# Optimization experiments

Measured on AMD Instinct MI355X. Metric: run time of the kernel, lower is better.

## Reference

```python
import jax, jax.numpy as jnp
import numpy as np

D_MODEL = 1024
N_EXPERTS = 8
D_FF = 4096
B, S = 2, 2048
INIT_SCALE = 0.02


def setup_inputs() -> dict:
    key = jax.random.key(0)
    ks = jax.random.split(key, 8)
    x = jax.random.normal(ks[0], (B, S, D_MODEL), dtype=jnp.float32)
    gate_w = jax.random.normal(ks[1], (D_MODEL, N_EXPERTS), dtype=jnp.float32) * INIT_SCALE
    gate_b = jnp.zeros((N_EXPERTS,), dtype=jnp.float32)
    w1 = jax.random.normal(ks[2], (N_EXPERTS, D_MODEL, D_FF), dtype=jnp.float32) * INIT_SCALE
    b1 = jnp.zeros((N_EXPERTS, D_FF), dtype=jnp.float32)
    w2 = jax.random.normal(ks[3], (N_EXPERTS, D_FF, D_MODEL), dtype=jnp.float32) * INIT_SCALE
    b2 = jnp.zeros((N_EXPERTS, D_MODEL), dtype=jnp.float32)
    return {"x": x, "gate_w": gate_w, "gate_b": gate_b,
            "w1": w1, "b1": b1, "w2": w2, "b2": b2}


def reference(x, gate_w, gate_b, w1, b1, w2, b2):
    E = w1.shape[0]
    # --- Top2Router ---
    logits = x @ gate_w + gate_b                      # [B,S,E]
    scores = jax.nn.softmax(logits, axis=-1)          # [B,S,E]
    val, idx = jax.lax.top_k(scores, 2)               # [B,S,2]
    # scatter top-2 softmax values into a dense [B,S,E] dispatch mask
    dispatch = (jax.nn.one_hot(idx, E, dtype=scores.dtype) * val[..., None]).sum(axis=-2)
    expert_counts = dispatch.sum(axis=(0, 1))         # [E]
    # --- dense loop over experts (vectorized over E), masked combine ---
    # h: [B,E,S,d_ff]
    h = jax.nn.gelu(jnp.einsum('bsd,edf->besf', x, w1) + b1[None, :, None, :],
                    approximate=False)
    y = jnp.einsum('besf,efd->besd', h, w2) + b2[None, :, None, :]  # [B,E,S,D]
    out = jnp.einsum('besd,bse->bsd', y, dispatch)    # masked sum over experts
    return out, dispatch, expert_counts
```

## Files before the change

### kernel.cpp

```cpp
#include <hip/hip_runtime.h>
#include <hip/hip_bf16.h>
#include <math.h>

#define DM    1024
#define NE    8
#define DF    4096
#define NT    4096
#define RCAP  9216
#define OUT_N   (NT*DM)
#define DISP_N  (NT*NE)
#define TOTAL_OUT (OUT_N + DISP_N + NE)

typedef __attribute__((ext_vector_type(4))) float f32x4;
typedef __attribute__((ext_vector_type(8))) short bf16x8;

#define WS_CNT    0
#define WS_FILL   32
#define WS_OFFS   64
#define WS_TOK    128
#define WS_WGT    (WS_TOK + RCAP*4)
#define WS_TOPE   (WS_WGT + RCAP*4)
#define WS_TOPV   (WS_TOPE + NT*2*4)
#define WS_W1T    (((WS_TOPV + NT*2*4) + 255) & ~255ul)
#define WS_W2T    (WS_W1T + (size_t)NE*DF*DM*2)
#define WS_XG     (WS_W2T + (size_t)NE*DM*DF*2)
#define WS_H      (WS_XG  + (size_t)RCAP*DM*2)

__device__ __forceinline__ void async_copy16(const __hip_bfloat16* g, __hip_bfloat16* l) {
    __builtin_amdgcn_global_load_lds(
        (const __attribute__((address_space(1))) unsigned int*)g,
        (__attribute__((address_space(3))) unsigned int*)l, 16, 0, 0);
}

__global__ void init_kernel(float* __restrict__ out, int* __restrict__ cnt,
                            int* __restrict__ fill, int* __restrict__ tok) {
    int gid = blockIdx.x * blockDim.x + threadIdx.x;
    int stride = gridDim.x * blockDim.x;
    for (int i = gid; i < TOTAL_OUT; i += stride) out[i] = 0.0f;
    if (gid < RCAP) tok[gid] = -1;
    if (gid < NE) { cnt[gid] = 0; fill[gid] = 0; }
}

__global__ void transpose_cast(const float* __restrict__ in, __hip_bfloat16* __restrict__ outp,
                               int R, int C) {
    __shared__ float tile[32][33];
    int e = blockIdx.z;
    int c0 = blockIdx.x * 32, r0 = blockIdx.y * 32;
    const float* ib = in + (size_t)e * R * C;
    __hip_bfloat16* ob = outp + (size_t)e * R * C;
    int tx = threadIdx.x & 31, ty = threadIdx.x >> 5;
    for (int rr = ty; rr < 32; rr += 8)
        tile[rr][tx] = ib[(size_t)(r0 + rr) * C + c0 + tx];
    __syncthreads();
    for (int cc = ty; cc < 32; cc += 8)
        ob[(size_t)(c0 + cc) * R + r0 + tx] = __float2bfloat16(tile[tx][cc]);
}

__global__ void gate_kernel(const float* __restrict__ x, const float* __restrict__ gw,
                            const float* __restrict__ gb, float* __restrict__ disp,
                            float* __restrict__ counts, int* __restrict__ cnt,
                            int* __restrict__ tope, float* __restrict__ topv) {
    int t = blockIdx.x;
    int l = threadIdx.x;
    const float* xr = x + (size_t)t * DM;
    double p[NE];
    #pragma unroll
    for (int e = 0; e < NE; ++e) p[e] = 0.0;
    for (int i = 0; i < DM / 64; ++i) {
        int d = l + 64 * i;
        double xv = (double)xr[d];
        const float* gr = gw + (size_t)d * NE;
        #pragma unroll
        for (int e = 0; e < NE; ++e) p[e] += xv * (double)gr[e];
    }
    #pragma unroll
    for (int off = 32; off > 0; off >>= 1) {
        #pragma unroll
        for (int e = 0; e < NE; ++e) p[e] += __shfl_xor(p[e], off, 64);
    }
    if (l == 0) {
        double lg[NE];
        double m = -1e300;
        #pragma unroll
        for (int e = 0; e < NE; ++e) { lg[e] = p[e] + (double)gb[e]; m = fmax(m, lg[e]); }
        double s = 0.0;
        #pragma unroll
        for (int e = 0; e < NE; ++e) s += exp(lg[e] - m);
        int e1 = 0;
        #pragma unroll
        for (int e = 1; e < NE; ++e) if (lg[e] > lg[e1]) e1 = e;
        int e2 = (e1 == 0) ? 1 : 0;
        #pragma unroll
        for (int e = 0; e < NE; ++e) if (e != e1 && lg[e] > lg[e2]) e2 = e;
        float v1 = (float)(exp(lg[e1] - m) / s);
        float v2 = (float)(exp(lg[e2] - m) / s);
        float* dr = disp + (size_t)t * NE;
        #pragma unroll
        for (int e = 0; e < NE; ++e) dr[e] = 0.0f;
        dr[e1] = v1; dr[e2] = v2;
        atomicAdd(&counts[e1], v1);
        atomicAdd(&counts[e2], v2);
        atomicAdd(&cnt[e1], 1);
        atomicAdd(&cnt[e2], 1);
        tope[2 * t] = e1;     topv[2 * t] = v1;
        tope[2 * t + 1] = e2; topv[2 * t + 1] = v2;
    }
}

__global__ void scan_kernel(const int* __restrict__ cnt, int* __restrict__ offs) {
    if (threadIdx.x == 0 && blockIdx.x == 0) {
        int o = 0;
        for (int e = 0; e < NE; ++e) {
            offs[e] = o;
            o += (cnt[e] + 127) & ~127;
        }
        offs[NE] = o;
    }
}

__global__ void build_kernel(const int* __restrict__ tope, const float* __restrict__ topv,
                             const int* __restrict__ offs, int* __restrict__ fill,
                             int* __restrict__ tok, float* __restrict__ wgt) {
    int t = blockIdx.x * blockDim.x + threadIdx.x;
    if (t >= NT) return;
    #pragma unroll
    for (int s = 0; s < 2; ++s) {
        int e = tope[2 * t + s];
        int pos = atomicAdd(&fill[e], 1);
        int row = offs[e] + pos;
        tok[row] = t;
        wgt[row] = topv[2 * t + s];
    }
}

__global__ void gather_kernel(const float* __restrict__ x, const int* __restrict__ tok,
                              __hip_bfloat16* __restrict__ xg) {
    int row = blockIdx.x;
    int t = tok[row];
    if (t < 0) return;
    int i = threadIdx.x;
    const float4 v = ((const float4*)(x + (size_t)t * DM))[i];
    ushort4 o;
    o.x = __bfloat16_as_ushort(__float2bfloat16(v.x));
    o.y = __bfloat16_as_ushort(__float2bfloat16(v.y));
    o.z = __bfloat16_as_ushort(__float2bfloat16(v.z));
    o.w = __bfloat16_as_ushort(__float2bfloat16(v.w));
    ((ushort4*)(xg + (size_t)row * DM))[i] = o;
}


__global__ __launch_bounds__(256) void gemm1_kernel(
    const __hip_bfloat16* __restrict__ xg, const __hip_bfloat16* __restrict__ w1t,
    const float* __restrict__ b1, __hip_bfloat16* __restrict__ h,
    const int* __restrict__ offs, const int* __restrict__ cnt) {
    __shared__ __hip_bfloat16 As[128 * 32];
    __shared__ __hip_bfloat16 Bs[128 * 32];
    const int row0 = blockIdx.y * 128;
    const int total = offs[NE];
    if (row0 >= total) return;
    int e = 0;
    while (row0 >= offs[e + 1]) ++e;
    if (row0 >= offs[e] + cnt[e]) return;
    const int n0 = blockIdx.x * 128;
    const __hip_bfloat16* Ab = xg + (size_t)row0 * DM;
    const __hip_bfloat16* Bb = w1t + (size_t)e * DF * DM + (size_t)n0 * DM;

    const int tid = threadIdx.x, lane = tid & 63, wave = tid >> 6;
    const int wm = wave >> 1, wn = wave & 1, g = lane >> 4, r = lane & 15;
    const int c1 = tid, c2 = tid + 256;

    f32x4 acc[4][4];
    #pragma unroll
    for (int m = 0; m < 4; ++m)
        #pragma unroll
        for (int n = 0; n < 4; ++n)
            #pragma unroll
            for (int j = 0; j < 4; ++j) acc[m][n][j] = 0.0f;

    for (int k0 = 0; k0 < DM; k0 += 32) {
        async_copy16(Ab + (size_t)(c1 >> 2) * DM + k0 + (c1 & 3) * 8, As + c1 * 8);
        async_copy16(Ab + (size_t)(c2 >> 2) * DM + k0 + (c2 & 3) * 8, As + c2 * 8);
        async_copy16(Bb + (size_t)(c1 >> 2) * DM + k0 + (c1 & 3) * 8, Bs + c1 * 8);
        async_copy16(Bb + (size_t)(c2 >> 2) * DM + k0 + (c2 & 3) * 8, Bs + c2 * 8);
        __syncthreads();
        bf16x8 af[4], bfr[4];
        #pragma unroll
        for (int m = 0; m < 4; ++m)
            af[m] = *(const bf16x8*)(As + (wm * 64 + m * 16 + r) * 32 + g * 8);
        #pragma unroll
        for (int n = 0; n < 4; ++n)
            bfr[n] = *(const bf16x8*)(Bs + (wn * 64 + n * 16 + r) * 32 + g * 8);
        #pragma unroll
        for (int m = 0; m < 4; ++m)
            #pragma unroll
            for (int n = 0; n < 4; ++n)
                acc[m][n] = __builtin_amdgcn_mfma_f32_16x16x32_bf16(af[m], bfr[n], acc[m][n], 0, 0, 0);
        __syncthreads();
    }
    float bb[4];
    #pragma unroll
    for (int n = 0; n < 4; ++n) bb[n] = b1[(size_t)e * DF + n0 + wn * 64 + n * 16 + r];
    #pragma unroll
    for (int m = 0; m < 4; ++m) {
        #pragma unroll
        for (int i = 0; i < 4; ++i) {
            int rowi = row0 + wm * 64 + m * 16 + g * 4 + i;
            __hip_bfloat16* hr = h + (size_t)rowi * DF + n0 + wn * 64 + r;
            #pragma unroll
            for (int n = 0; n < 4; ++n) {
                float v = acc[m][n][i] + bb[n];
                float ge = 0.5f * v * (1.0f + erff(v * 0.70710678118654752f));
                hr[n * 16] = __float2bfloat16(ge);
            }
        }
    }
}

__global__ __launch_bounds__(256) void gemm2_kernel(
    const __hip_bfloat16* __restrict__ h, const __hip_bfloat16* __restrict__ w2t,
    const float* __restrict__ b2, float* __restrict__ out,
    const int* __restrict__ offs, const int* __restrict__ cnt,
    const int* __restrict__ tok, const float* __restrict__ wgt) {
    __shared__ __hip_bfloat16 As[128 * 32];
    __shared__ __hip_bfloat16 Bs[128 * 32];
    const int row0 = blockIdx.y * 128;
    const int total = offs[NE];
    if (row0 >= total) return;
    int e = 0;
    while (row0 >= offs[e + 1]) ++e;
    if (row0 >= offs[e] + cnt[e]) return;
    const int n0 = blockIdx.x * 128;
    const __hip_bfloat16* Ab = h + (size_t)row0 * DF;
    const __hip_bfloat16* Bb = w2t + (size_t)e * DM * DF + (size_t)n0 * DF;

    const int tid = threadIdx.x, lane = tid & 63, wave = tid >> 6;
    const int wm = wave >> 1, wn = wave & 1, g = lane >> 4, r = lane & 15;
    const int c1 = tid, c2 = tid + 256;

    f32x4 acc[4][4];
    #pragma unroll
    for (int m = 0; m < 4; ++m)
        #pragma unroll
        for (int n = 0; n < 4; ++n)
            #pragma unroll
            for (int j = 0; j < 4; ++j) acc[m][n][j] = 0.0f;

    for (int k0 = 0; k0 < DF; k0 += 32) {
        async_copy16(Ab + (size_t)(c1 >> 2) * DF + k0 + (c1 & 3) * 8, As + c1 * 8);
        async_copy16(Ab + (size_t)(c2 >> 2) * DF + k0 + (c2 & 3) * 8, As + c2 * 8);
        async_copy16(Bb + (size_t)(c1 >> 2) * DF + k0 + (c1 & 3) * 8, Bs + c1 * 8);
        async_copy16(Bb + (size_t)(c2 >> 2) * DF + k0 + (c2 & 3) * 8, Bs + c2 * 8);
        __syncthreads();
        bf16x8 af[4], bfr[4];
        #pragma unroll
        for (int m = 0; m < 4; ++m)
            af[m] = *(const bf16x8*)(As + (wm * 64 + m * 16 + r) * 32 + g * 8);
        #pragma unroll
        for (int n = 0; n < 4; ++n)
            bfr[n] = *(const bf16x8*)(Bs + (wn * 64 + n * 16 + r) * 32 + g * 8);
        #pragma unroll
        for (int m = 0; m < 4; ++m)
            #pragma unroll
            for (int n = 0; n < 4; ++n)
                acc[m][n] = __builtin_amdgcn_mfma_f32_16x16x32_bf16(af[m], bfr[n], acc[m][n], 0, 0, 0);
        __syncthreads();
    }
    float bb[4];
    #pragma unroll
    for (int n = 0; n < 4; ++n) bb[n] = b2[(size_t)e * DM + n0 + wn * 64 + n * 16 + r];
    #pragma unroll
    for (int m = 0; m < 4; ++m) {
        #pragma unroll
        for (int i = 0; i < 4; ++i) {
            int rowi = row0 + wm * 64 + m * 16 + g * 4 + i;
            int t = tok[rowi];
            if (t < 0) continue;
            float wv = wgt[rowi];
            float* orow = out + (size_t)t * DM + n0 + wn * 64 + r;
            #pragma unroll
            for (int n = 0; n < 4; ++n)
                atomicAdd(orow + n * 16, wv * (acc[m][n][i] + bb[n]));
        }
    }
}

extern "C" void kernel_launch(void* const* d_in, const int* in_sizes, int n_in,
                              void* d_out, int out_size, void* d_ws, size_t ws_size,
                              hipStream_t stream) {
    const float* x  = (const float*)d_in[0];
    const float* gw = (const float*)d_in[1];
    const float* gb = (const float*)d_in[2];
    const float* w1 = (const float*)d_in[3];
    const float* b1 = (const float*)d_in[4];
    const float* w2 = (const float*)d_in[5];
    const float* b2 = (const float*)d_in[6];

    float* out    = (float*)d_out;
    float* disp   = out + OUT_N;
    float* counts = disp + DISP_N;

    char* ws = (char*)d_ws;
    int*   cnt  = (int*)(ws + WS_CNT);
    int*   fill = (int*)(ws + WS_FILL);
    int*   offs = (int*)(ws + WS_OFFS);
    int*   tok  = (int*)(ws + WS_TOK);
    float* wgt  = (float*)(ws + WS_WGT);
    int*   tope = (int*)(ws + WS_TOPE);
    float* topv = (float*)(ws + WS_TOPV);
    __hip_bfloat16* w1t = (__hip_bfloat16*)(ws + WS_W1T);
    __hip_bfloat16* w2t = (__hip_bfloat16*)(ws + WS_W2T);
    __hip_bfloat16* xg  = (__hip_bfloat16*)(ws + WS_XG);
    __hip_bfloat16* h   = (__hip_bfloat16*)(ws + WS_H);

    init_kernel<<<4096, 256, 0, stream>>>(out, cnt, fill, tok);
    transpose_cast<<<dim3(DF / 32, DM / 32, NE), 256, 0, stream>>>(w1, w1t, DM, DF);
    transpose_cast<<<dim3(DM / 32, DF / 32, NE), 256, 0, stream>>>(w2, w2t, DF, DM);
    gate_kernel<<<NT, 64, 0, stream>>>(x, gw, gb, disp, counts, cnt, tope, topv);
    scan_kernel<<<1, 64, 0, stream>>>(cnt, offs);
    build_kernel<<<NT / 256, 256, 0, stream>>>(tope, topv, offs, fill, tok, wgt);
    gather_kernel<<<RCAP, 256, 0, stream>>>(x, tok, xg);
    gemm1_kernel<<<dim3(DF / 128, RCAP / 128), 256, 0, stream>>>(xg, w1t, b1, h, offs, cnt);
    gemm2_kernel<<<dim3(DM / 128, RCAP / 128), 256, 0, stream>>>(h, w2t, b2, out, offs, cnt, tok, wgt);
}
```

Measured before the change: 786.0 us.

## Widen weight transpose tiles, split-K gemm2, remap workgroups, use tanh GELU

The weight transpose-cast now uses 64x64 tiles, float4 loads and ushort4 stores, and converts to bf16 before writing to LDS. gemm1 and gemm2 use a 1D grid with a workgroup remap that spreads neighbouring blocks across 8 groups, likely for XCD/L2 locality. gemm2 splits K four ways and accumulates into the output with atomics, giving more blocks and parallelism at the cost of four times the atomic traffic. The exact erf GELU is replaced by the tanh approximation, which slightly changes numerics.

```diff
diff --git a/kernel.cpp b/kernel.cpp
--- a/kernel.cpp
+++ b/kernel.cpp
@@ -32,6 +32,13 @@
         (__attribute__((address_space(3))) unsigned int*)l, 16, 0, 0);
 }
 
+__device__ __forceinline__ float gelu_f(float v) {
+    float u = v * (0.7978845608028654f + 0.044715f * 0.7978845608028654f * v * v);
+    float t = __expf(2.0f * u);
+    float th = 1.0f - 2.0f / (t + 1.0f);
+    return 0.5f * v * (1.0f + th);
+}
+
 __global__ void init_kernel(float* __restrict__ out, int* __restrict__ cnt,
                             int* __restrict__ fill, int* __restrict__ tok) {
     int gid = blockIdx.x * blockDim.x + threadIdx.x;
@@ -41,19 +48,30 @@
     if (gid < NE) { cnt[gid] = 0; fill[gid] = 0; }
 }
 
-__global__ void transpose_cast(const float* __restrict__ in, __hip_bfloat16* __restrict__ outp,
-                               int R, int C) {
-    __shared__ float tile[32][33];
+__global__ __launch_bounds__(256) void transpose_cast2(const float* __restrict__ in,
+                                                       __hip_bfloat16* __restrict__ outp,
+                                                       int R, int C) {
+    __shared__ ushort tile[64][72];
     int e = blockIdx.z;
-    int c0 = blockIdx.x * 32, r0 = blockIdx.y * 32;
+    int c0 = blockIdx.x * 64, r0 = blockIdx.y * 64;
     const float* ib = in + (size_t)e * R * C;
-    __hip_bfloat16* ob = outp + (size_t)e * R * C;
-    int tx = threadIdx.x & 31, ty = threadIdx.x >> 5;
-    for (int rr = ty; rr < 32; rr += 8)
-        tile[rr][tx] = ib[(size_t)(r0 + rr) * C + c0 + tx];
+    ushort* ob = (ushort*)outp + (size_t)e * R * C;
+    int tx = threadIdx.x & 15, ty = threadIdx.x >> 4;
+    #pragma unroll
+    for (int j = 0; j < 4; ++j) {
+        int row = ty + 16 * j;
+        float4 v = *(const float4*)(ib + (size_t)(r0 + row) * C + c0 + tx * 4);
+        tile[tx * 4 + 0][row] = __bfloat16_as_ushort(__float2bfloat16(v.x));
+        tile[tx * 4 + 1][row] = __bfloat16_as_ushort(__float2bfloat16(v.y));
+        tile[tx * 4 + 2][row] = __bfloat16_as_ushort(__float2bfloat16(v.z));
+        tile[tx * 4 + 3][row] = __bfloat16_as_ushort(__float2bfloat16(v.w));
+    }
     __syncthreads();
-    for (int cc = ty; cc < 32; cc += 8)
-        ob[(size_t)(c0 + cc) * R + r0 + tx] = __float2bfloat16(tile[tx][cc]);
+    #pragma unroll
+    for (int j = 0; j < 4; ++j) {
+        int cc = ty + 16 * j;
+        *(ushort4*)(ob + (size_t)(c0 + cc) * R + r0 + tx * 4) = *(const ushort4*)&tile[cc][tx * 4];
+    }
 }
 
 __global__ void gate_kernel(const float* __restrict__ x, const float* __restrict__ gw,
@@ -155,13 +173,18 @@
     const int* __restrict__ offs, const int* __restrict__ cnt) {
     __shared__ __hip_bfloat16 As[128 * 32];
     __shared__ __hip_bfloat16 Bs[128 * 32];
-    const int row0 = blockIdx.y * 128;
+    const int NXT = DF / 128;
+    const int nwg = NXT * (RCAP / 128);
+    int wg = (int)blockIdx.x;
+    int id = (wg & 7) * (nwg >> 3) + (wg >> 3);
+    const int bx = id % NXT, by = id / NXT;
+    const int row0 = by * 128;
     const int total = offs[NE];
     if (row0 >= total) return;
     int e = 0;
     while (row0 >= offs[e + 1]) ++e;
     if (row0 >= offs[e] + cnt[e]) return;
-    const int n0 = blockIdx.x * 128;
+    const int n0 = bx * 128;
     const __hip_bfloat16* Ab = xg + (size_t)row0 * DM;
     const __hip_bfloat16* Bb = w1t + (size_t)e * DF * DM + (size_t)n0 * DM;
 
@@ -207,15 +230,13 @@
             int rowi = row0 + wm * 64 + m * 16 + g * 4 + i;
             __hip_bfloat16* hr = h + (size_t)rowi * DF + n0 + wn * 64 + r;
             #pragma unroll
-            for (int n = 0; n < 4; ++n) {
-                float v = acc[m][n][i] + bb[n];
-                float ge = 0.5f * v * (1.0f + erff(v * 0.70710678118654752f));
-                hr[n * 16] = __float2bfloat16(ge);
-            }
+            for (int n = 0; n < 4; ++n)
+                hr[n * 16] = __float2bfloat16(gelu_f(acc[m][n][i] + bb[n]));
         }
     }
 }
 
+#define KSP 4
 __global__ __launch_bounds__(256) void gemm2_kernel(
     const __hip_bfloat16* __restrict__ h, const __hip_bfloat16* __restrict__ w2t,
     const float* __restrict__ b2, float* __restrict__ out,
@@ -223,13 +244,20 @@
     const int* __restrict__ tok, const float* __restrict__ wgt) {
     __shared__ __hip_bfloat16 As[128 * 32];
     __shared__ __hip_bfloat16 Bs[128 * 32];
-    const int row0 = blockIdx.y * 128;
+    const int NXT = DM / 128;
+    const int nwg = NXT * (RCAP / 128) * KSP;
+    int wg = (int)blockIdx.x;
+    int id = (wg & 7) * (nwg >> 3) + (wg >> 3);
+    const int bx = id & 7;
+    const int ksp = (id >> 3) & (KSP - 1);
+    const int by = id >> 5;
+    const int row0 = by * 128;
     const int total = offs[NE];
     if (row0 >= total) return;
     int e = 0;
     while (row0 >= offs[e + 1]) ++e;
     if (row0 >= offs[e] + cnt[e]) return;
-    const int n0 = blockIdx.x * 128;
+    const int n0 = bx * 128;
     const __hip_bfloat16* Ab = h + (size_t)row0 * DF;
     const __hip_bfloat16* Bb = w2t + (size_t)e * DM * DF + (size_t)n0 * DF;
 
@@ -245,7 +273,8 @@
             #pragma unroll
             for (int j = 0; j < 4; ++j) acc[m][n][j] = 0.0f;
 
-    for (int k0 = 0; k0 < DF; k0 += 32) {
+    const int kbeg = ksp * (DF / KSP), kend = kbeg + DF / KSP;
+    for (int k0 = kbeg; k0 < kend; k0 += 32) {
         async_copy16(Ab + (size_t)(c1 >> 2) * DF + k0 + (c1 & 3) * 8, As + c1 * 8);
         async_copy16(Ab + (size_t)(c2 >> 2) * DF + k0 + (c2 & 3) * 8, As + c2 * 8);
         async_copy16(Bb + (size_t)(c1 >> 2) * DF + k0 + (c1 & 3) * 8, Bs + c1 * 8);
@@ -267,7 +296,8 @@
     }
     float bb[4];
     #pragma unroll
-    for (int n = 0; n < 4; ++n) bb[n] = b2[(size_t)e * DM + n0 + wn * 64 + n * 16 + r];
+    for (int n = 0; n < 4; ++n)
+        bb[n] = (ksp == 0) ? b2[(size_t)e * DM + n0 + wn * 64 + n * 16 + r] : 0.0f;
     #pragma unroll
     for (int m = 0; m < 4; ++m) {
         #pragma unroll
@@ -313,12 +343,12 @@
     __hip_bfloat16* h   = (__hip_bfloat16*)(ws + WS_H);
 
     init_kernel<<<4096, 256, 0, stream>>>(out, cnt, fill, tok);
-    transpose_cast<<<dim3(DF / 32, DM / 32, NE), 256, 0, stream>>>(w1, w1t, DM, DF);
-    transpose_cast<<<dim3(DM / 32, DF / 32, NE), 256, 0, stream>>>(w2, w2t, DF, DM);
+    transpose_cast2<<<dim3(DF / 64, DM / 64, NE), 256, 0, stream>>>(w1, w1t, DM, DF);
+    transpose_cast2<<<dim3(DM / 64, DF / 64, NE), 256, 0, stream>>>(w2, w2t, DF, DM);
     gate_kernel<<<NT, 64, 0, stream>>>(x, gw, gb, disp, counts, cnt, tope, topv);
     scan_kernel<<<1, 64, 0, stream>>>(cnt, offs);
     build_kernel<<<NT / 256, 256, 0, stream>>>(tope, topv, offs, fill, tok, wgt);
     gather_kernel<<<RCAP, 256, 0, stream>>>(x, tok, xg);
-    gemm1_kernel<<<dim3(DF / 128, RCAP / 128), 256, 0, stream>>>(xg, w1t, b1, h, offs, cnt);
-    gemm2_kernel<<<dim3(DM / 128, RCAP / 128), 256, 0, stream>>>(h, w2t, b2, out, offs, cnt, tok, wgt);
-}
+    gemm1_kernel<<<(DF / 128) * (RCAP / 128), 256, 0, stream>>>(xg, w1t, b1, h, offs, cnt);
+    gemm2_kernel<<<(DM / 128) * (RCAP / 128) * KSP, 256, 0, stream>>>(h, w2t, b2, out, offs, cnt, tok, wgt);
+}
```

After: 770.8 us. Within noise of the previous version (-1.9%).
